# Optimization experiments

Hardware: AMD Instinct MI355X
Metric: run time of the kernel (lower is better)

Reference implementation:

```python
import jax, jax.numpy as jnp
import numpy as np

N = 50000      # nodes
C = 64         # in_channels
O = 64         # out_channels (== in_channels, required by zeros_like in original)
S = 8          # size: number of weight matrices
E = 1700000    # edges (neighbor pairs incl. self-loops), avg degree ~34


def setup_inputs() -> dict:
    key = jax.random.key(0)
    ks = jax.random.split(key, 9)
    node_tensor = jax.random.normal(ks[0], (N, C), dtype=jnp.float32)
    src = jax.random.randint(ks[1], (E,), 0, N)                 # neighbor node j
    dst = jnp.sort(jax.random.randint(ks[2], (E,), 0, N))       # center node i
    sc = 1.0 / np.sqrt(C)
    W = jax.random.normal(ks[3], (S, C, O), dtype=jnp.float32) * sc   # linears weights
    b = jax.random.normal(ks[4], (S, O), dtype=jnp.float32) * sc      # linears biases
    Ws = jax.random.normal(ks[5], (C, S), dtype=jnp.float32) * sc     # source proj
    bs = jax.random.normal(ks[6], (S,), dtype=jnp.float32) * sc
    Wt = jax.random.normal(ks[7], (C, S), dtype=jnp.float32) * sc     # target proj
    bt = jax.random.normal(ks[8], (S,), dtype=jnp.float32) * sc
    return dict(node_tensor=node_tensor, src=src, dst=dst,
                W=W, b=b, Ws=Ws, bs=bs, Wt=Wt, bt=bt)


def reference(node_tensor, src, dst, W, b, Ws, bs, Wt, bt):
    # Per-node soft-assignment logits (FeaStNet)
    s = node_tensor @ Ws + bs          # [N, S] : source_tensor
    t = node_tensor @ Wt + bt          # [N, S] : target_tensor
    # Per-edge assignment: softmax over the `size` dim of source[center] + target[neighbor]
    q = jax.nn.softmax(s[dst] + t[src], axis=-1)      # [E, S]
    # Per-matrix projected node features: weighted[m] = x @ W_m + b_m
    Wx = jnp.einsum('nc,sco->sno', node_tensor, W) + b[:, None, :]   # [S, N, O]
    # msg[e] = sum_m q[e,m] * Wx[m, src[e]]; loop over small fixed S to avoid [S,E,O] blowup
    msg = q[:, 0:1] * Wx[0][src]                      # [E, O]
    for m in range(1, S):
        msg = msg + q[:, m:m + 1] * Wx[m][src]
    # Scatter-sum over each center's neighborhood, mean over the S weight matrices
    out = jax.ops.segment_sum(msg, dst, num_segments=N) / S          # [N, O]
    return out
```

## Files before the change

kernel.cpp:

```cpp
#include <hip/hip_runtime.h>
#include <hip/hip_bf16.h>


#define CDIM 64
#define SDIM 8

typedef __bf16 bf16x8 __attribute__((ext_vector_type(8)));
typedef __bf16 bf16x4 __attribute__((ext_vector_type(4)));
typedef float f32x4 __attribute__((ext_vector_type(4)));

__global__ __launch_bounds__(256) void k1_pre(
    const float* __restrict__ x, const float* __restrict__ Ws,
    const float* __restrict__ bs, const float* __restrict__ Wt,
    const float* __restrict__ bt, const float* __restrict__ W,
    const int* __restrict__ dst, float* __restrict__ ST,
    __hip_bfloat16* __restrict__ xbf, __hip_bfloat16* __restrict__ WtB,
    int* __restrict__ rowptr, int N, int E, int nbN) {
  int bid = blockIdx.x;
  if (bid >= nbN + 128) {
    int e = (bid - nbN - 128) * 256 + threadIdx.x;
    if (e >= E) return;
    int a = dst[e];
    int bnd = (e + 1 < E) ? dst[e + 1] : N;
    if (e == 0) {
      for (int d = 0; d <= a; ++d) rowptr[d] = 0;
    }
    for (int d = a + 1; d <= bnd; ++d) rowptr[d] = e + 1;
    return;
  }
  if (bid >= nbN) {
    int t = (bid - nbN) * 256 + threadIdx.x;
    int o = t >> 9, k = t & 511;
    WtB[t] = __float2bfloat16(W[(size_t)k * 64 + o]);
    return;
  }

  __shared__ __hip_bfloat16 wst[16 * 72];
  __shared__ float bst[16];
  int t = threadIdx.x;
#pragma unroll
  for (int j = 0; j < 4; ++j) {
    int idx = t * 4 + j;
    int n = idx >> 6, k = idx & 63;
    float v = (n < 8) ? Ws[k * 8 + n] : Wt[k * 8 + (n - 8)];
    wst[n * 72 + k] = __float2bfloat16(v);
  }
  if (t < 16) bst[t] = (t < 8) ? bs[t] : bt[t - 8];
  __syncthreads();

  int wave = t >> 6, lane = t & 63;
  int r = lane & 15, q = lane >> 4;
  int node = bid * 64 + wave * 16 + r;
  int nodec = node < N ? node : N - 1;
  const float* xr = x + (size_t)nodec * CDIM;

  bf16x8 afrag[2];
#pragma unroll
  for (int kt = 0; kt < 2; ++kt) {
    float4 u0 = *(const float4*)(xr + kt * 32 + q * 8);
    float4 u1 = *(const float4*)(xr + kt * 32 + q * 8 + 4);
    union { bf16x8 v; __hip_bfloat16 h[8]; } a;
    a.h[0] = __float2bfloat16(u0.x); a.h[1] = __float2bfloat16(u0.y);
    a.h[2] = __float2bfloat16(u0.z); a.h[3] = __float2bfloat16(u0.w);
    a.h[4] = __float2bfloat16(u1.x); a.h[5] = __float2bfloat16(u1.y);
    a.h[6] = __float2bfloat16(u1.z); a.h[7] = __float2bfloat16(u1.w);
    afrag[kt] = a.v;
    if (node < N)
      *(bf16x8*)(xbf + (size_t)node * CDIM + kt * 32 + q * 8) = a.v;
  }

  bf16x8 bf0 = *(const bf16x8*)(wst + r * 72 + q * 8);
  bf16x8 bf1 = *(const bf16x8*)(wst + r * 72 + 32 + q * 8);

  f32x4 acc = {0, 0, 0, 0};
  acc = __builtin_amdgcn_mfma_f32_16x16x32_bf16(afrag[0], bf0, acc, 0, 0, 0);
  acc = __builtin_amdgcn_mfma_f32_16x16x32_bf16(afrag[1], bf1, acc, 0, 0, 0);

  int m = lane & 15;
#pragma unroll
  for (int v = 0; v < 4; ++v) {
    int nd = bid * 64 + wave * 16 + q * 4 + v;
    if (nd >= N) continue;
    float val = acc[v] + bst[m];
    if (m >= 8) val = __expf(val);
    ST[nd * 16 + m] = val;
  }
}

__global__ __launch_bounds__(256, 4) void k3_mfma(
    const __hip_bfloat16* __restrict__ xbf, const int* __restrict__ src,
    const int* __restrict__ rowptr, const float* __restrict__ ST,
    __hip_bfloat16* __restrict__ Gbf, float* __restrict__ R, int N) {
  __shared__ __hip_bfloat16 qt_s[4][16 * 40];
  __shared__ __hip_bfloat16 xt_s[4][4 * 32 * 16];

  int wave = threadIdx.x >> 6;
  int lane = threadIdx.x & 63;
  int i = blockIdx.x * 4 + wave;
  if (i >= N) return;

  int mm = lane & 7;
  int kk = lane >> 3;
  int mp = lane & 15;
  int q3 = lane >> 4;

  __hip_bfloat16* qt = &qt_s[wave][0];
  __hip_bfloat16* xt = &xt_s[wave][0];

  __hip_bfloat16 z0 = __float2bfloat16(0.0f);
#pragma unroll
  for (int z = 0; z < 5; ++z) qt[320 + z * 64 + lane] = z0;

  int lo = rowptr[i];
  int hi = rowptr[i + 1];
  float uv = __expf(ST[i * 16 + mm]);

  unsigned rd_addr = (unsigned)(uintptr_t)xt + (unsigned)q3 * 256u +
                     (unsigned)mp * 8u;
  __hip_bfloat16* xw = xt + (mm >> 1) * 512 + (mm & 1) * 8;

  f32x4 acc0 = {0, 0, 0, 0}, acc1 = {0, 0, 0, 0};
  f32x4 acc2 = {0, 0, 0, 0}, acc3 = {0, 0, 0, 0};
  float racc = 0.f;

  if (lo < hi) {
    int ecl = hi - 1;
    int iv[4], niv[4];
    bf16x8 xv[4];
    float tv[4];

#pragma unroll
    for (int g = 0; g < 4; ++g) {
      int ek = lo + g * 8 + kk;
      iv[g] = src[ek < ecl ? ek : ecl];
    }
#pragma unroll
    for (int g = 0; g < 4; ++g)
      xv[g] = *(const bf16x8*)(xbf + (size_t)iv[g] * CDIM + mm * 8);
#pragma unroll
    for (int g = 0; g < 4; ++g) tv[g] = ST[iv[g] * 16 + 8 + mm];
    if (lo + 32 < hi) {
#pragma unroll
      for (int g = 0; g < 4; ++g) {
        int ek = lo + 32 + g * 8 + kk;
        niv[g] = src[ek < ecl ? ek : ecl];
      }
    }

    for (int c0 = lo; c0 < hi; c0 += 32) {
      bool hasn = (c0 + 32 < hi);
      bf16x8 nxv[4];
      float ntv[4];
      int nniv[4];
      if (hasn) {
#pragma unroll
        for (int g = 0; g < 4; ++g)
          nxv[g] = *(const bf16x8*)(xbf + (size_t)niv[g] * CDIM + mm * 8);
#pragma unroll
        for (int g = 0; g < 4; ++g) ntv[g] = ST[niv[g] * 16 + 8 + mm];
        if (c0 + 64 < hi) {
#pragma unroll
          for (int g = 0; g < 4; ++g) {
            int ek = c0 + 64 + g * 8 + kk;
            nniv[g] = src[ek < ecl ? ek : ecl];
          }
        }
      }

#pragma unroll
      for (int g = 0; g < 4; ++g) {
        float w = uv * tv[g];
        float ssum = w + __shfl_xor(w, 1);
        ssum += __shfl_xor(ssum, 2);
        ssum += __shfl_xor(ssum, 4);
        float qv = w * __frcp_rn(ssum);
        if (c0 + g * 8 + kk >= hi) qv = 0.f;
        racc += qv;
        qt[mm * 40 + g * 8 + kk] = __float2bfloat16(qv);
      }

#pragma unroll
      for (int g = 0; g < 4; ++g)
        *(bf16x8*)(xw + (g * 8 + kk) * 16) = xv[g];

      bf16x8 afrag = *(const bf16x8*)(qt + mp * 40 + q3 * 8);

      bf16x4 t0, t1, t2, t3, t4, t5, t6, t7;
      asm volatile(
          "ds_read_b64_tr_b16 %0, %8 offset:0\n\t"
          "ds_read_b64_tr_b16 %1, %8 offset:128\n\t"
          "ds_read_b64_tr_b16 %2, %8 offset:1024\n\t"
          "ds_read_b64_tr_b16 %3, %8 offset:1152\n\t"
          "ds_read_b64_tr_b16 %4, %8 offset:2048\n\t"
          "ds_read_b64_tr_b16 %5, %8 offset:2176\n\t"
          "ds_read_b64_tr_b16 %6, %8 offset:3072\n\t"
          "ds_read_b64_tr_b16 %7, %8 offset:3200"
          : "=&v"(t0), "=&v"(t1), "=&v"(t2), "=&v"(t3),
            "=&v"(t4), "=&v"(t5), "=&v"(t6), "=&v"(t7)
          : "v"(rd_addr)
          : "memory");
      asm volatile("s_waitcnt lgkmcnt(0)" ::: "memory");
      __builtin_amdgcn_sched_barrier(0);

      union { bf16x8 v; bf16x4 h[2]; } b0, b1, b2, b3;
      b0.h[0] = t0; b0.h[1] = t1;
      b1.h[0] = t2; b1.h[1] = t3;
      b2.h[0] = t4; b2.h[1] = t5;
      b3.h[0] = t6; b3.h[1] = t7;

      acc0 = __builtin_amdgcn_mfma_f32_16x16x32_bf16(afrag, b0.v, acc0, 0, 0, 0);
      acc1 = __builtin_amdgcn_mfma_f32_16x16x32_bf16(afrag, b1.v, acc1, 0, 0, 0);
      acc2 = __builtin_amdgcn_mfma_f32_16x16x32_bf16(afrag, b2.v, acc2, 0, 0, 0);
      acc3 = __builtin_amdgcn_mfma_f32_16x16x32_bf16(afrag, b3.v, acc3, 0, 0, 0);

      if (hasn) {
#pragma unroll
        for (int g = 0; g < 4; ++g) {
          iv[g] = niv[g];
          xv[g] = nxv[g];
          tv[g] = ntv[g];
          niv[g] = nniv[g];
        }
      }
    }
  }

  if (q3 < 2) {
    __hip_bfloat16* Gi = Gbf + (size_t)i * 512;
#pragma unroll
    for (int v = 0; v < 4; ++v) {
      int m = q3 * 4 + v;
      Gi[m * 64 + 0 + mp]  = __float2bfloat16(acc0[v]);
      Gi[m * 64 + 16 + mp] = __float2bfloat16(acc1[v]);
      Gi[m * 64 + 32 + mp] = __float2bfloat16(acc2[v]);
      Gi[m * 64 + 48 + mp] = __float2bfloat16(acc3[v]);
    }
  }

  racc += __shfl_xor(racc, 8);
  racc += __shfl_xor(racc, 16);
  racc += __shfl_xor(racc, 32);
  if (lane < 8) R[(size_t)i * 8 + lane] = racc;
}

__global__ __launch_bounds__(256) void k4_mfma(
    const __hip_bfloat16* __restrict__ Gbf, const float* __restrict__ R,
    const __hip_bfloat16* __restrict__ WtB, const float* __restrict__ bias,
    float* __restrict__ out, int N) {
  int wave = threadIdx.x >> 6;
  int lane = threadIdx.x & 63;
  int r0 = (blockIdx.x * 4 + wave) * 16;
  if (r0 >= N) return;

  int m = lane & 15;
  int q = lane >> 4;
  const __bf16* abase = (const __bf16*)(Gbf + (size_t)(r0 + m) * 512) + q * 8;
  const __bf16* wbase = (const __bf16*)WtB + (size_t)m * 512 + q * 8;

  f32x4 acc0 = {0, 0, 0, 0}, acc1 = {0, 0, 0, 0};
  f32x4 acc2 = {0, 0, 0, 0}, acc3 = {0, 0, 0, 0};
#pragma unroll
  for (int kt = 0; kt < 16; ++kt) {
    bf16x8 a = *(const bf16x8*)(abase + kt * 32);
    bf16x8 b0 = *(const bf16x8*)(wbase + 0 * 8192 + kt * 32);
    bf16x8 b1 = *(const bf16x8*)(wbase + 1 * 8192 + kt * 32);
    bf16x8 b2 = *(const bf16x8*)(wbase + 2 * 8192 + kt * 32);
    bf16x8 b3 = *(const bf16x8*)(wbase + 3 * 8192 + kt * 32);
    acc0 = __builtin_amdgcn_mfma_f32_16x16x32_bf16(a, b0, acc0, 0, 0, 0);
    acc1 = __builtin_amdgcn_mfma_f32_16x16x32_bf16(a, b1, acc1, 0, 0, 0);
    acc2 = __builtin_amdgcn_mfma_f32_16x16x32_bf16(a, b2, acc2, 0, 0, 0);
    acc3 = __builtin_amdgcn_mfma_f32_16x16x32_bf16(a, b3, acc3, 0, 0, 0);
  }

#pragma unroll
  for (int v = 0; v < 4; ++v) {
    int ri = r0 + q * 4 + v;
    if (ri >= N) continue;
    const float* Ri = R + (size_t)ri * 8;
    float b0s = 0, b1s = 0, b2s = 0, b3s = 0;
#pragma unroll
    for (int mm = 0; mm < 8; ++mm) {
      float rv = Ri[mm];
      b0s = fmaf(rv, bias[mm * 64 + 0 + m], b0s);
      b1s = fmaf(rv, bias[mm * 64 + 16 + m], b1s);
      b2s = fmaf(rv, bias[mm * 64 + 32 + m], b2s);
      b3s = fmaf(rv, bias[mm * 64 + 48 + m], b3s);
    }
    float* orow = out + (size_t)ri * 64;
    orow[0 + m]  = (acc0[v] + b0s) * 0.125f;
    orow[16 + m] = (acc1[v] + b1s) * 0.125f;
    orow[32 + m] = (acc2[v] + b2s) * 0.125f;
    orow[48 + m] = (acc3[v] + b3s) * 0.125f;
  }
}

extern "C" void kernel_launch(void* const* d_in, const int* in_sizes, int n_in,
                              void* d_out, int out_size, void* d_ws, size_t ws_size,
                              hipStream_t stream) {
  const float* x  = (const float*)d_in[0];
  const int* src  = (const int*)d_in[1];
  const int* dst  = (const int*)d_in[2];
  const float* W  = (const float*)d_in[3];
  const float* b  = (const float*)d_in[4];
  const float* Ws = (const float*)d_in[5];
  const float* bs = (const float*)d_in[6];
  const float* Wt = (const float*)d_in[7];
  const float* bt = (const float*)d_in[8];
  int N = in_sizes[0] / CDIM;
  int E = in_sizes[1];
  float* out = (float*)d_out;

  float* ST = (float*)d_ws;
  __hip_bfloat16* Gbf = (__hip_bfloat16*)(ST + (size_t)N * 16);
  float* R  = (float*)(Gbf + (size_t)N * 512);
  __hip_bfloat16* WtB = (__hip_bfloat16*)(R + (size_t)N * 8);
  __hip_bfloat16* xbf = WtB + 64 * 512;
  int* rowptr = (int*)(xbf + (size_t)N * CDIM);

  int nbN = (N + 63) / 64;
  int nbE = (E + 255) / 256;
  k1_pre<<<nbN + 128 + nbE, 256, 0, stream>>>(x, Ws, bs, Wt, bt, W, dst, ST,
                                              xbf, WtB, rowptr, N, E, nbN);
  k3_mfma<<<(N + 3) / 4, 256, 0, stream>>>(xbf, src, rowptr, ST, Gbf, R, N);
  int mtiles = (N + 15) / 16;
  k4_mfma<<<(mtiles + 3) / 4, 256, 0, stream>>>(Gbf, R, WtB, b, out, N);
}
```

Measured before the change: 182.5 us.

## Fuse neighborhood aggregation and output projection into one kernel via LDS

Merges the aggregation kernel and the output GEMM kernel. Each 512-thread block aggregates 8 nodes into a shared-memory G tile, then four waves run the 16x512x64 MFMA projection and bias epilogue straight from LDS. This drops the global round trip of the N×512 bf16 G buffer and the R buffer, plus one kernel launch. In exchange, half of each 16-row MFMA tile is zero padding, only 4 of 8 waves do the epilogue, and the added block-wide barrier and larger LDS footprint may lower occupancy.

```diff
diff --git a/kernel.cpp b/kernel.cpp
--- a/kernel.cpp
+++ b/kernel.cpp
@@ -87,17 +87,21 @@
   }
 }
 
-__global__ __launch_bounds__(256, 4) void k3_mfma(
+__global__ __launch_bounds__(512, 4) void k3_fused(
     const __hip_bfloat16* __restrict__ xbf, const int* __restrict__ src,
     const int* __restrict__ rowptr, const float* __restrict__ ST,
-    __hip_bfloat16* __restrict__ Gbf, float* __restrict__ R, int N) {
-  __shared__ __hip_bfloat16 qt_s[4][16 * 40];
-  __shared__ __hip_bfloat16 xt_s[4][4 * 32 * 16];
+    const __hip_bfloat16* __restrict__ WtB, const float* __restrict__ bias,
+    float* __restrict__ out, int N) {
+  __shared__ __hip_bfloat16 qt_s[8][16 * 40];
+  __shared__ __hip_bfloat16 xt_s[8][4 * 32 * 16];
+  __shared__ __hip_bfloat16 Gs[16 * 520];
+  __shared__ float Rs[8][8];
 
   int wave = threadIdx.x >> 6;
   int lane = threadIdx.x & 63;
-  int i = blockIdx.x * 4 + wave;
-  if (i >= N) return;
+  int i0 = blockIdx.x * 8;
+  int i = i0 + wave;
+  bool valid = i < N;
 
   int mm = lane & 7;
   int kk = lane >> 3;
@@ -111,9 +115,12 @@
 #pragma unroll
   for (int z = 0; z < 5; ++z) qt[320 + z * 64 + lane] = z0;
 
-  int lo = rowptr[i];
-  int hi = rowptr[i + 1];
-  float uv = __expf(ST[i * 16 + mm]);
+  int lo = 0, hi = 0;
+  if (valid) {
+    lo = rowptr[i];
+    hi = rowptr[i + 1];
+  }
+  float uv = __expf(ST[(size_t)(valid ? i : 0) * 16 + mm]);
 
   unsigned rd_addr = (unsigned)(uintptr_t)xt + (unsigned)q3 * 256u +
                      (unsigned)mp * 8u;
@@ -226,7 +233,7 @@
   }
 
   if (q3 < 2) {
-    __hip_bfloat16* Gi = Gbf + (size_t)i * 512;
+    __hip_bfloat16* Gi = Gs + wave * 520;
 #pragma unroll
     for (int v = 0; v < 4; ++v) {
       int m = q3 * 4 + v;
@@ -236,61 +243,50 @@
       Gi[m * 64 + 48 + mp] = __float2bfloat16(acc3[v]);
     }
   }
+  {
+    union { bf16x8 v; __hip_bfloat16 h[8]; } zz;
+#pragma unroll
+    for (int j = 0; j < 8; ++j) zz.h[j] = z0;
+    *(bf16x8*)(Gs + (8 + wave) * 520 + lane * 8) = zz.v;
+  }
 
   racc += __shfl_xor(racc, 8);
   racc += __shfl_xor(racc, 16);
   racc += __shfl_xor(racc, 32);
-  if (lane < 8) R[(size_t)i * 8 + lane] = racc;
-}
-
-__global__ __launch_bounds__(256) void k4_mfma(
-    const __hip_bfloat16* __restrict__ Gbf, const float* __restrict__ R,
-    const __hip_bfloat16* __restrict__ WtB, const float* __restrict__ bias,
-    float* __restrict__ out, int N) {
-  int wave = threadIdx.x >> 6;
-  int lane = threadIdx.x & 63;
-  int r0 = (blockIdx.x * 4 + wave) * 16;
-  if (r0 >= N) return;
-
-  int m = lane & 15;
-  int q = lane >> 4;
-  const __bf16* abase = (const __bf16*)(Gbf + (size_t)(r0 + m) * 512) + q * 8;
-  const __bf16* wbase = (const __bf16*)WtB + (size_t)m * 512 + q * 8;
-
-  f32x4 acc0 = {0, 0, 0, 0}, acc1 = {0, 0, 0, 0};
-  f32x4 acc2 = {0, 0, 0, 0}, acc3 = {0, 0, 0, 0};
-#pragma unroll
-  for (int kt = 0; kt < 16; ++kt) {
-    bf16x8 a = *(const bf16x8*)(abase + kt * 32);
-    bf16x8 b0 = *(const bf16x8*)(wbase + 0 * 8192 + kt * 32);
-    bf16x8 b1 = *(const bf16x8*)(wbase + 1 * 8192 + kt * 32);
-    bf16x8 b2 = *(const bf16x8*)(wbase + 2 * 8192 + kt * 32);
-    bf16x8 b3 = *(const bf16x8*)(wbase + 3 * 8192 + kt * 32);
-    acc0 = __builtin_amdgcn_mfma_f32_16x16x32_bf16(a, b0, acc0, 0, 0, 0);
-    acc1 = __builtin_amdgcn_mfma_f32_16x16x32_bf16(a, b1, acc1, 0, 0, 0);
-    acc2 = __builtin_amdgcn_mfma_f32_16x16x32_bf16(a, b2, acc2, 0, 0, 0);
-    acc3 = __builtin_amdgcn_mfma_f32_16x16x32_bf16(a, b3, acc3, 0, 0, 0);
-  }
-
-#pragma unroll
-  for (int v = 0; v < 4; ++v) {
-    int ri = r0 + q * 4 + v;
-    if (ri >= N) continue;
-    const float* Ri = R + (size_t)ri * 8;
-    float b0s = 0, b1s = 0, b2s = 0, b3s = 0;
-#pragma unroll
-    for (int mm = 0; mm < 8; ++mm) {
-      float rv = Ri[mm];
-      b0s = fmaf(rv, bias[mm * 64 + 0 + m], b0s);
-      b1s = fmaf(rv, bias[mm * 64 + 16 + m], b1s);
-      b2s = fmaf(rv, bias[mm * 64 + 32 + m], b2s);
-      b3s = fmaf(rv, bias[mm * 64 + 48 + m], b3s);
-    }
-    float* orow = out + (size_t)ri * 64;
-    orow[0 + m]  = (acc0[v] + b0s) * 0.125f;
-    orow[16 + m] = (acc1[v] + b1s) * 0.125f;
-    orow[32 + m] = (acc2[v] + b2s) * 0.125f;
-    orow[48 + m] = (acc3[v] + b3s) * 0.125f;
+  if (lane < 8) Rs[wave][lane] = racc;
+
+  __syncthreads();
+
+  if (wave < 4) {
+    int ct = wave;
+    int m = lane & 15;
+    int q = lane >> 4;
+    const __bf16* abase = (const __bf16*)Gs + (size_t)m * 520 + q * 8;
+    const __bf16* wb = (const __bf16*)WtB + (size_t)(ct * 16 + m) * 512 + q * 8;
+
+    f32x4 eacc = {0, 0, 0, 0};
+#pragma unroll
+    for (int kt = 0; kt < 16; ++kt) {
+      bf16x8 a = *(const bf16x8*)(abase + kt * 32);
+      bf16x8 b = *(const bf16x8*)(wb + kt * 32);
+      eacc = __builtin_amdgcn_mfma_f32_16x16x32_bf16(a, b, eacc, 0, 0, 0);
+    }
+
+#pragma unroll
+    for (int v = 0; v < 4; ++v) {
+      int r = q * 4 + v;
+      if (r < 8) {
+        int node = i0 + r;
+        if (node < N) {
+          int o = ct * 16 + m;
+          float bsum = 0.f;
+#pragma unroll
+          for (int mb = 0; mb < 8; ++mb)
+            bsum = fmaf(Rs[r][mb], bias[mb * 64 + o], bsum);
+          out[(size_t)node * 64 + o] = (eacc[v] + bsum) * 0.125f;
+        }
+      }
+    }
   }
 }
 
@@ -311,9 +307,7 @@
   float* out = (float*)d_out;
 
   float* ST = (float*)d_ws;
-  __hip_bfloat16* Gbf = (__hip_bfloat16*)(ST + (size_t)N * 16);
-  float* R  = (float*)(Gbf + (size_t)N * 512);
-  __hip_bfloat16* WtB = (__hip_bfloat16*)(R + (size_t)N * 8);
+  __hip_bfloat16* WtB = (__hip_bfloat16*)(ST + (size_t)N * 16);
   __hip_bfloat16* xbf = WtB + 64 * 512;
   int* rowptr = (int*)(xbf + (size_t)N * CDIM);
 
@@ -321,7 +315,6 @@
   int nbE = (E + 255) / 256;
   k1_pre<<<nbN + 128 + nbE, 256, 0, stream>>>(x, Ws, bs, Wt, bt, W, dst, ST,
                                               xbf, WtB, rowptr, N, E, nbN);
-  k3_mfma<<<(N + 3) / 4, 256, 0, stream>>>(xbf, src, rowptr, ST, Gbf, R, N);
-  int mtiles = (N + 15) / 16;
-  k4_mfma<<<(mtiles + 3) / 4, 256, 0, stream>>>(Gbf, R, WtB, b, out, N);
+  k3_fused<<<(N + 7) / 8, 512, 0, stream>>>(xbf, src, rowptr, ST, WtB, b,
+                                            out, N);
 }
```

Result: slower. 209.2 us (+14.7%).
